# Performance work log

Measured on AMD Instinct MI355X. Metric: run time of the kernel, lower is better.

The kernel has to match this reference:

```python
import jax, jax.numpy as jnp
import numpy as np

RATIO_DENSE = 0.95   # ratio_th[-2] used for dense matching at conv5_2
RATIO_REFINE = 0.9   # ratio_th[k] used by refine_points
EPS = 1e-8
NEIGHBORS = jnp.array([[0, 0], [0, 1], [1, 0], [1, 1]])  # (x, y) offsets


def setup_inputs() -> dict:
    key = jax.random.key(0)
    k1, k2, k3, k4 = jax.random.split(key, 4)
    return {
        'map_A': jax.random.normal(k1, (1, 512, 96, 96), dtype=jnp.float32),
        'map_B': jax.random.normal(k2, (1, 512, 96, 96), dtype=jnp.float32),
        'act_A': jax.random.normal(k3, (1, 512, 192, 192), dtype=jnp.float32),
        'act_B': jax.random.normal(k4, (1, 512, 192, 192), dtype=jnp.float32),
    }


def _mnn_ratio_mask(sim, ratio):
    """Mutual-NN + ratio-test. sim: [N1, N2] cosine similarities.
    Returns nn12 [N1] (best match in B for each A) and boolean mask [N1]."""
    s12, i12 = jax.lax.top_k(sim, 2)            # [N1, 2]
    d12 = 2.0 - 2.0 * s12                       # cosine sim -> squared L2 dist
    r12 = d12[:, 0] / (d12[:, 1] + EPS)
    nn12 = i12[:, 0]
    s21, i21 = jax.lax.top_k(sim.T, 2)          # [N2, 2]
    d21 = 2.0 - 2.0 * s21
    r21 = d21[:, 0] / (d21[:, 1] + EPS)
    nn21 = i21[:, 0]
    ids1 = jnp.arange(sim.shape[0])
    mask = (ids1 == nn21[nn12]) & (r12 <= ratio) & (r21[nn12] <= ratio)
    return nn12, mask


def reference(map_A, map_B, act_A, act_B):
    ch = map_A.shape[1]
    hA, wA = map_A.shape[2], map_A.shape[3]
    hB, wB = map_B.shape[2], map_B.shape[3]

    # ---- dense_feature_matching (padded / masked form) ----
    d1 = map_A.reshape(ch, -1).T               # [N1, ch]
    d1 = d1 / jnp.linalg.norm(d1, axis=1, keepdims=True)
    d2 = map_B.reshape(ch, -1).T               # [N2, ch]
    d2 = d2 / jnp.linalg.norm(d2, axis=1, keepdims=True)
    sim = d1 @ d2.T                            # [N1, N2], the big one
    nn12, valid = _mnn_ratio_mask(sim, RATIO_DENSE)

    idx = jnp.arange(hA * wA)
    yA, xA = jnp.divmod(idx, wA)
    yB, xB = jnp.divmod(nn12, wB)
    border = ((xA == 0) | (xA == wA - 1) | (yA == 0) | (yA == hA - 1) |
              (xB == 0) | (xB == wB - 1) | (yB == 0) | (yB == hB - 1))
    valid = valid & ~border
    # pad invalid points to (0,0) so refine gathers stay in-bounds
    pA = jnp.stack([jnp.where(valid, xA, 0), jnp.where(valid, yA, 0)])  # [2, P]
    pB = jnp.stack([jnp.where(valid, xB, 0), jnp.where(valid, yB, 0)])

    # ---- refine_points (fully vectorized gather-dot-topk over all P points) ----
    dA = act_A[0] / jnp.sqrt(jnp.sum(act_A[0] ** 2, axis=0, keepdims=True))
    dB = act_B[0] / jnp.sqrt(jnp.sum(act_B[0] ** 2, axis=0, keepdims=True))
    pA2 = pA * 2
    pB2 = pB * 2
    P = pA.shape[1]

    gAx = pA2[0][:, None] + NEIGHBORS[:, 0][None, :]   # [P, 4]
    gAy = pA2[1][:, None] + NEIGHBORS[:, 1][None, :]
    gBx = pB2[0][:, None] + NEIGHBORS[:, 0][None, :]
    gBy = pB2[1][:, None] + NEIGHBORS[:, 1][None, :]
    actAg = dA[:, gAy, gAx]                            # [ch, P, 4]
    actBg = dB[:, gBy, gBx]                            # [ch, P, 4]
    scores = jnp.einsum('cpi,cpj->pij', actAg, actBg)  # [P, 4, 4]

    sA, mA = jax.lax.top_k(scores, 2)                  # [P, 4, 2]
    sA = 2.0 - 2.0 * sA
    ratio_A2B = sA[..., 0] / (sA[..., 1] + EPS)        # [P, 4]
    match_A2B = mA[..., 0]
    score_A2B = sA[..., 0]

    sB, mB = jax.lax.top_k(jnp.swapaxes(scores, 1, 2), 2)
    sB = 2.0 - 2.0 * sB
    ratio_B2A = sB[..., 0] / (sB[..., 1] + EPS)
    match_B2A = mB[..., 0]

    ar = jnp.arange(P)
    ind_A = (ar[:, None] * 4 + match_A2B).reshape(-1)  # [P*4]
    ind_B = (ar[:, None] * 4 + match_B2A).reshape(-1)
    ind = jnp.arange(P * 4)
    mask = (jnp.minimum(ratio_A2B, ratio_B2A) < RATIO_REFINE) & \
           (ind_B[ind_A] == ind).reshape(P, 4)

    # drop the two worst (largest-distance) neighbor candidates per point
    score_masked = jnp.where(mask, score_A2B, 5.0)
    _, discard = jax.lax.top_k(score_masked, 2)
    mask = mask.at[ar, discard[:, 0]].set(False)
    mask = mask.at[ar, discard[:, 1]].set(False)
    mask = mask & valid[:, None]

    refined_A = jnp.stack([gAx, gAy])                                   # [2, P, 4]
    rBx = pB2[0][:, None] + NEIGHBORS[:, 0][match_A2B]
    rBy = pB2[1][:, None] + NEIGHBORS[:, 1][match_A2B]
    refined_B = jnp.stack([rBx, rBy])                                   # [2, P, 4]

    return refined_A, refined_B, mask, scores
```

## Files before the change

### kernel.cpp

```cpp
#include <hip/hip_runtime.h>
#include <stdint.h>

#define CH 512
#define W1 96
#define P1 (W1*W1)
#define W2 192
#define P2 (W2*W2)
#define BM 256
#define BN 256
#define NTT 36
#define BK 32
#define NKS (CH/BK)
#define EPSF 1e-8f
#define RDENSE 0.95f
#define RREFINE 0.9f

typedef __attribute__((ext_vector_type(8))) short bf16x8_t;
typedef __attribute__((ext_vector_type(4))) float f32x4_t;

__device__ __forceinline__ unsigned enc_f32(float f){
  unsigned u = __float_as_uint(f);
  return (u & 0x80000000u) ? ~u : (u | 0x80000000u);
}
__device__ __forceinline__ float dec_f32(unsigned e){
  unsigned u = (e & 0x80000000u) ? (e & 0x7FFFFFFFu) : ~e;
  return __uint_as_float(u);
}
__device__ __forceinline__ unsigned long long packVI(float v, int idx){
  return (((unsigned long long)enc_f32(v)) << 32) | (unsigned)(~(unsigned)idx);
}
__device__ __forceinline__ float packedVal(unsigned long long p){ return dec_f32((unsigned)(p >> 32)); }
__device__ __forceinline__ int packedIdx(unsigned long long p){ return (int)(~(unsigned)(p & 0xFFFFFFFFull)); }
__device__ __forceinline__ void merge2(unsigned long long &b, unsigned long long &s, unsigned long long c){
  if (c > b){ s = b; b = c; } else if (c > s){ s = c; }
}

__device__ __forceinline__ unsigned short f2bf(float f){
  unsigned u = __float_as_uint(f);
  unsigned r = (u + 0x7FFFu + ((u >> 16) & 1u)) >> 16;
  return (unsigned short)r;
}

__device__ __forceinline__ void gload16(const void* g, void* l){
  __builtin_amdgcn_global_load_lds(
      (const __attribute__((address_space(1))) unsigned int*)g,
      (__attribute__((address_space(3))) unsigned int*)l, 16, 0, 0);
}

__global__ void desc_norm(const float* __restrict__ mA, const float* __restrict__ mB,
                          float* __restrict__ inv1, float* __restrict__ inv2){
  int p = blockIdx.x * blockDim.x + threadIdx.x;
  const float* m = (p < P1) ? mA : mB;
  float* o = (p < P1) ? inv1 : inv2;
  int pix = (p < P1) ? p : p - P1;
  float s = 0.f;
  for (int c = 0; c < CH; ++c){ float v = m[c*P1 + pix]; s += v*v; }
  o[pix] = 1.0f / sqrtf(s);
}

__global__ void act_norm(const float* __restrict__ aA, const float* __restrict__ aB,
                         float* __restrict__ invA, float* __restrict__ invB){
  int p = blockIdx.x * blockDim.x + threadIdx.x;
  const float* m = (p < P2) ? aA : aB;
  float* o = (p < P2) ? invA : invB;
  int pix = (p < P2) ? p : p - P2;
  float s = 0.f;
  for (int c = 0; c < CH; ++c){ float v = m[c*P2 + pix]; s += v*v; }
  o[pix] = 1.0f / sqrtf(s);
}

__global__ __launch_bounds__(256)
void prep_split(const float* __restrict__ src, const float* __restrict__ inv,
                unsigned short* __restrict__ hi, unsigned short* __restrict__ lo){
  __shared__ float tile[64][65];
  const int pixBase = blockIdx.x * 64;
  const int chBase  = blockIdx.y * 64;
  const int t = threadIdx.x;
  #pragma unroll
  for (int rep = 0; rep < 16; ++rep){
    int idx = rep*256 + t;
    int c = idx >> 6, p = idx & 63;
    tile[c][p] = src[(chBase + c)*P1 + pixBase + p];
  }
  __syncthreads();
  const int p = t >> 2, cg = (t & 3) * 16;
  const float iv = inv[pixBase + p];
  unsigned short hbuf[16], lbuf[16];
  #pragma unroll
  for (int j = 0; j < 16; ++j){
    float v = tile[cg + j][p] * iv;
    unsigned short h = f2bf(v);
    float hv = __uint_as_float((unsigned)h << 16);
    unsigned short l2 = f2bf(v - hv);
    hbuf[j] = h; lbuf[j] = l2;
  }
  size_t off = (size_t)(pixBase + p) * CH + chBase + cg;
  *(uint4*)(hi + off)     = ((const uint4*)hbuf)[0];
  *(uint4*)(hi + off + 8) = ((const uint4*)hbuf)[1];
  *(uint4*)(lo + off)     = ((const uint4*)lbuf)[0];
  *(uint4*)(lo + off + 8) = ((const uint4*)lbuf)[1];
}

__global__ __launch_bounds__(512, 2)
void sim_mfma(const unsigned short* __restrict__ Ah, const unsigned short* __restrict__ Al,
              const unsigned short* __restrict__ Bh, const unsigned short* __restrict__ Bl,
              unsigned long long* __restrict__ rowCand,
              unsigned long long* __restrict__ colCand){
  __shared__ __align__(16) char lds[131072];

  const int nwg = NTT*NTT;
  int bid = blockIdx.x;
  int swz = (bid & 7) * (nwg >> 3) + (bid >> 3);
  const int rt = swz / NTT, ct = swz % NTT;
  const int rBase = rt * BM, cBase = ct * BN;

  const int t = threadIdx.x;
  const int w = t >> 6, lane = t & 63;
  const int wr = w >> 2, wc = w & 3;
  const int l15 = lane & 15, lj = lane >> 4;

  const int panel = w >> 1, sub = w & 1;
  const unsigned short* gpan = (panel == 0) ? (Ah + (size_t)rBase*CH)
                             : (panel == 1) ? (Al + (size_t)rBase*CH)
                             : (panel == 2) ? (Bh + (size_t)cBase*CH)
                                            : (Bl + (size_t)cBase*CH);
  int gOff[8];
  #pragma unroll
  for (int i = 0; i < 8; ++i){
    int slot = sub*512 + i*64 + lane;
    int row = slot >> 2, chkp = slot & 3;
    int chk = chkp ^ ((row >> 1) & 3);
    gOff[i] = row * (CH*2) + chk * 16;
  }
  const int ldsPanelOff = panel*16384 + sub*8192;

  int aOff[8], bOff[4];
  #pragma unroll
  for (int mi = 0; mi < 8; ++mi){
    int rA = wr*128 + mi*16 + l15;
    aOff[mi] = rA*64 + ((lj ^ ((rA >> 1) & 3)) << 4);
  }
  #pragma unroll
  for (int ni = 0; ni < 4; ++ni){
    int rB = wc*64 + ni*16 + l15;
    bOff[ni] = rB*64 + ((lj ^ ((rB >> 1) & 3)) << 4);
  }

  f32x4_t acc[8][4];
  #pragma unroll
  for (int i = 0; i < 8; ++i)
    #pragma unroll
    for (int j = 0; j < 4; ++j)
      #pragma unroll
      for (int r = 0; r < 4; ++r) acc[i][j][r] = 0.f;

  {
    const char* gb = (const char*)gpan;
    #pragma unroll
    for (int i = 0; i < 8; ++i)
      gload16(gb + gOff[i], lds + ldsPanelOff + i*1024);
  }
  __syncthreads();

  for (int ks = 0; ks < NKS; ++ks){
    const int cur = ks & 1;
    if (ks + 1 < NKS){
      const char* gb = (const char*)gpan + (ks+1)*BK*2;
      #pragma unroll
      for (int i = 0; i < 8; ++i)
        gload16(gb + gOff[i], lds + (cur^1)*65536 + ldsPanelOff + i*1024);
    }
    const char* bp = lds + cur*65536;
    bf16x8_t ahf[8], alf[8];
    #pragma unroll
    for (int mi = 0; mi < 8; ++mi){
      ahf[mi] = *(const bf16x8_t*)(bp + aOff[mi]);
      alf[mi] = *(const bf16x8_t*)(bp + 16384 + aOff[mi]);
    }
    #pragma unroll
    for (int ni = 0; ni < 4; ++ni){
      bf16x8_t bhf = *(const bf16x8_t*)(bp + 32768 + bOff[ni]);
      bf16x8_t blf = *(const bf16x8_t*)(bp + 49152 + bOff[ni]);
      #pragma unroll
      for (int mi = 0; mi < 8; ++mi){
        acc[mi][ni] = __builtin_amdgcn_mfma_f32_16x16x32_bf16(ahf[mi], bhf, acc[mi][ni], 0, 0, 0);
        acc[mi][ni] = __builtin_amdgcn_mfma_f32_16x16x32_bf16(ahf[mi], blf, acc[mi][ni], 0, 0, 0);
        acc[mi][ni] = __builtin_amdgcn_mfma_f32_16x16x32_bf16(alf[mi], bhf, acc[mi][ni], 0, 0, 0);
      }
    }
    __syncthreads();
  }

  unsigned long long (*rowScr)[4][2] = (unsigned long long (*)[4][2])(lds);
  unsigned long long (*colScr)[2][2] = (unsigned long long (*)[2][2])(lds + 16384);

  #pragma unroll
  for (int mi = 0; mi < 8; ++mi){
    #pragma unroll
    for (int reg = 0; reg < 4; ++reg){
      unsigned long long b = 0ull, s = 0ull;
      #pragma unroll
      for (int ni = 0; ni < 4; ++ni){
        int col = cBase + wc*64 + ni*16 + l15;
        merge2(b, s, packVI(acc[mi][ni][reg], col));
      }
      #pragma unroll
      for (int m = 1; m < 16; m <<= 1){
        unsigned long long ob = __shfl_xor(b, m, 64);
        unsigned long long os = __shfl_xor(s, m, 64);
        merge2(b, s, ob); merge2(b, s, os);
      }
      if (l15 == 0){
        int rowLoc = wr*128 + mi*16 + lj*4 + reg;
        rowScr[rowLoc][wc][0] = b; rowScr[rowLoc][wc][1] = s;
      }
    }
  }
  #pragma unroll
  for (int ni = 0; ni < 4; ++ni){
    unsigned long long b = 0ull, s = 0ull;
    #pragma unroll
    for (int mi = 0; mi < 8; ++mi)
      #pragma unroll
      for (int reg = 0; reg < 4; ++reg){
        int row = rBase + wr*128 + mi*16 + lj*4 + reg;
        merge2(b, s, packVI(acc[mi][ni][reg], row));
      }
    #pragma unroll
    for (int m = 16; m < 64; m <<= 1){
      unsigned long long ob = __shfl_xor(b, m, 64);
      unsigned long long os = __shfl_xor(s, m, 64);
      merge2(b, s, ob); merge2(b, s, os);
    }
    if (lj == 0){
      int colLoc = wc*64 + ni*16 + l15;
      colScr[colLoc][wr][0] = b; colScr[colLoc][wr][1] = s;
    }
  }
  __syncthreads();
  if (t < 256){
    unsigned long long b = 0ull, s = 0ull;
    #pragma unroll
    for (int j = 0; j < 4; ++j){ merge2(b, s, rowScr[t][j][0]); merge2(b, s, rowScr[t][j][1]); }
    rowCand[((long long)ct*P1 + rBase + t)*2 + 0] = b;
    rowCand[((long long)ct*P1 + rBase + t)*2 + 1] = s;
  } else {
    int c = t - 256;
    unsigned long long b = 0ull, s = 0ull;
    #pragma unroll
    for (int j = 0; j < 2; ++j){ merge2(b, s, colScr[c][j][0]); merge2(b, s, colScr[c][j][1]); }
    colCand[((long long)rt*P1 + cBase + c)*2 + 0] = b;
    colCand[((long long)rt*P1 + cBase + c)*2 + 1] = s;
  }
}

__global__ void merge_cand(const unsigned long long* __restrict__ cand,
                           unsigned long long* __restrict__ top,
                           unsigned long long* __restrict__ sec){
  int p = blockIdx.x * blockDim.x + threadIdx.x;
  unsigned long long b = 0ull, s = 0ull;
  for (int tile = 0; tile < NTT; ++tile){
    merge2(b, s, cand[((long long)tile*P1 + p)*2 + 0]);
    merge2(b, s, cand[((long long)tile*P1 + p)*2 + 1]);
  }
  top[p] = b; sec[p] = s;
}

__global__ void match_k(const unsigned long long* __restrict__ rowTop,
                        const unsigned long long* __restrict__ rowSec,
                        const unsigned long long* __restrict__ colTop,
                        const unsigned long long* __restrict__ colSec,
                        int4* __restrict__ pts, int* __restrict__ validArr){
  int p = blockIdx.x * blockDim.x + threadIdx.x;
  unsigned long long rT = rowTop[p], rS = rowSec[p];
  float s0 = packedVal(rT), s1 = packedVal(rS);
  int nn12 = packedIdx(rT);
  float r12 = (2.f - 2.f*s0) / (2.f - 2.f*s1 + EPSF);
  unsigned long long cT = colTop[nn12], cS = colSec[nn12];
  int nn21 = packedIdx(cT);
  float r21 = (2.f - 2.f*packedVal(cT)) / (2.f - 2.f*packedVal(cS) + EPSF);
  int xA = p % W1, yA = p / W1, xB = nn12 % W1, yB = nn12 / W1;
  bool border = (xA==0)||(xA==W1-1)||(yA==0)||(yA==W1-1)||
                (xB==0)||(xB==W1-1)||(yB==0)||(yB==W1-1);
  bool valid = (nn21 == p) && (r12 <= RDENSE) && (r21 <= RDENSE) && !border;
  pts[p] = valid ? make_int4(xA,yA,xB,yB) : make_int4(0,0,0,0);
  validArr[p] = valid ? 1 : 0;
}

__global__ __launch_bounds__(256)
void refine(const float* __restrict__ actA, const float* __restrict__ actB,
            const float* __restrict__ invA, const float* __restrict__ invB,
            const int4* __restrict__ pts, float* __restrict__ scoresOut){
  int p = (blockIdx.x * blockDim.x + threadIdx.x) >> 6;
  int lane = threadIdx.x & 63;
  int4 q = pts[p];
  const int nbx[4] = {0,0,1,1}, nby[4] = {0,1,0,1};
  int offA[4], offB[4];
  #pragma unroll
  for (int i = 0; i < 4; ++i){
    offA[i] = (2*q.y + nby[i])*W2 + 2*q.x + nbx[i];
    offB[i] = (2*q.w + nby[i])*W2 + 2*q.z + nbx[i];
  }
  float acc[16] = {};
  #pragma unroll
  for (int k = 0; k < 8; ++k){
    int c = lane + 64*k;
    int base = c * P2;
    float a0 = actA[base+offA[0]], a1 = actA[base+offA[1]],
          a2 = actA[base+offA[2]], a3 = actA[base+offA[3]];
    float b0 = actB[base+offB[0]], b1 = actB[base+offB[1]],
          b2 = actB[base+offB[2]], b3 = actB[base+offB[3]];
    acc[ 0] = fmaf(a0,b0,acc[ 0]); acc[ 1] = fmaf(a0,b1,acc[ 1]);
    acc[ 2] = fmaf(a0,b2,acc[ 2]); acc[ 3] = fmaf(a0,b3,acc[ 3]);
    acc[ 4] = fmaf(a1,b0,acc[ 4]); acc[ 5] = fmaf(a1,b1,acc[ 5]);
    acc[ 6] = fmaf(a1,b2,acc[ 6]); acc[ 7] = fmaf(a1,b3,acc[ 7]);
    acc[ 8] = fmaf(a2,b0,acc[ 8]); acc[ 9] = fmaf(a2,b1,acc[ 9]);
    acc[10] = fmaf(a2,b2,acc[10]); acc[11] = fmaf(a2,b3,acc[11]);
    acc[12] = fmaf(a3,b0,acc[12]); acc[13] = fmaf(a3,b1,acc[13]);
    acc[14] = fmaf(a3,b2,acc[14]); acc[15] = fmaf(a3,b3,acc[15]);
  }
  #pragma unroll
  for (int m = 1; m < 64; m <<= 1)
    #pragma unroll
    for (int u = 0; u < 16; ++u) acc[u] += __shfl_xor(acc[u], m, 64);
  if (lane == 0){
    float sA[4], sB[4];
    #pragma unroll
    for (int i = 0; i < 4; ++i){ sA[i] = invA[offA[i]]; sB[i] = invB[offB[i]]; }
    float4* o = (float4*)(scoresOut + p*16);
    #pragma unroll
    for (int i = 0; i < 4; ++i)
      o[i] = make_float4(acc[i*4+0]*sA[i]*sB[0], acc[i*4+1]*sA[i]*sB[1],
                         acc[i*4+2]*sA[i]*sB[2], acc[i*4+3]*sA[i]*sB[3]);
  }
}

__global__ void final_k(const float* __restrict__ scores, const int4* __restrict__ pts,
                        const int* __restrict__ validArr, float* __restrict__ out){
  int p = blockIdx.x * blockDim.x + threadIdx.x;
  float sc[16];
  #pragma unroll
  for (int u = 0; u < 16; ++u) sc[u] = scores[p*16 + u];

  int matchA[4]; float ratioA[4], scoreA[4];
  #pragma unroll
  for (int i = 0; i < 4; ++i){
    int bi = 0; float bv = sc[i*4];
    #pragma unroll
    for (int j = 1; j < 4; ++j) if (sc[i*4+j] > bv){ bv = sc[i*4+j]; bi = j; }
    float sv = -3.402823466e38f;
    #pragma unroll
    for (int j = 0; j < 4; ++j) if (j != bi && sc[i*4+j] > sv){ sv = sc[i*4+j]; }
    matchA[i] = bi;
    float d0 = 2.f - 2.f*bv, d1 = 2.f - 2.f*sv;
    ratioA[i] = d0 / (d1 + EPSF); scoreA[i] = d0;
  }
  int matchB[4]; float ratioB[4];
  #pragma unroll
  for (int j = 0; j < 4; ++j){
    int bi = 0; float bv = sc[j];
    #pragma unroll
    for (int i = 1; i < 4; ++i) if (sc[i*4+j] > bv){ bv = sc[i*4+j]; bi = i; }
    float sv = -3.402823466e38f;
    #pragma unroll
    for (int i = 0; i < 4; ++i) if (i != bi && sc[i*4+j] > sv){ sv = sc[i*4+j]; }
    matchB[j] = bi;
    float d0 = 2.f - 2.f*bv, d1 = 2.f - 2.f*sv;
    ratioB[j] = d0 / (d1 + EPSF);
  }
  bool m[4];
  #pragma unroll
  for (int i = 0; i < 4; ++i)
    m[i] = (fminf(ratioA[i], ratioB[i]) < RREFINE) && (matchB[matchA[i]] == i);
  float smk[4];
  #pragma unroll
  for (int i = 0; i < 4; ++i) smk[i] = m[i] ? scoreA[i] : 5.0f;
  int d0i = 0; float d0v = smk[0];
  #pragma unroll
  for (int i = 1; i < 4; ++i) if (smk[i] > d0v){ d0v = smk[i]; d0i = i; }
  int d1i = -1; float d1v = -3.402823466e38f;
  #pragma unroll
  for (int i = 0; i < 4; ++i) if (i != d0i && smk[i] > d1v){ d1v = smk[i]; d1i = i; }
  m[d0i] = false; m[d1i] = false;
  bool v = validArr[p] != 0;
  int4 q = pts[p];
  const int nbx[4] = {0,0,1,1}, nby[4] = {0,1,0,1};
  #pragma unroll
  for (int i = 0; i < 4; ++i){
    out[           p*4 + i] = (float)(2*q.x + nbx[i]);
    out[  P1*4   + p*4 + i] = (float)(2*q.y + nby[i]);
    out[2*P1*4   + p*4 + i] = (float)(2*q.z + nbx[matchA[i]]);
    out[3*P1*4   + p*4 + i] = (float)(2*q.w + nby[matchA[i]]);
    out[4*P1*4   + p*4 + i] = (m[i] && v) ? 1.0f : 0.0f;
  }
}

extern "C" void kernel_launch(void* const* d_in, const int* in_sizes, int n_in,
                              void* d_out, int out_size, void* d_ws, size_t ws_size,
                              hipStream_t stream) {
  const float* mapA = (const float*)d_in[0];
  const float* mapB = (const float*)d_in[1];
  const float* actA = (const float*)d_in[2];
  const float* actB = (const float*)d_in[3];
  float* out = (float*)d_out;

  unsigned short* Ah = (unsigned short*)d_ws;
  unsigned short* Al = Ah + (size_t)P1*CH;
  unsigned short* Bh = Al + (size_t)P1*CH;
  unsigned short* Bl = Bh + (size_t)P1*CH;
  unsigned long long* rowCand = (unsigned long long*)(Bl + (size_t)P1*CH);
  unsigned long long* colCand = rowCand + (size_t)NTT*P1*2;
  unsigned long long* rowTop  = colCand + (size_t)NTT*P1*2;
  unsigned long long* rowSec  = rowTop + P1;
  unsigned long long* colTop  = rowSec + P1;
  unsigned long long* colSec  = colTop + P1;
  float* inv1 = (float*)(colSec + P1);
  float* inv2 = inv1 + P1;
  float* invA = inv2 + P1;
  float* invB = invA + P2;
  int4*  pts  = (int4*)(invB + P2);
  int*   validArr = (int*)(pts + P1);

  float* scoresOut = out + 4*P1*4 + P1*4;

  desc_norm <<<2*P1/256, 256, 0, stream>>>(mapA, mapB, inv1, inv2);
  act_norm  <<<2*P2/256, 256, 0, stream>>>(actA, actB, invA, invB);
  prep_split<<<dim3(P1/64, CH/64), 256, 0, stream>>>(mapA, inv1, Ah, Al);
  prep_split<<<dim3(P1/64, CH/64), 256, 0, stream>>>(mapB, inv2, Bh, Bl);
  sim_mfma  <<<NTT*NTT, 512, 0, stream>>>(Ah, Al, Bh, Bl, rowCand, colCand);
  merge_cand<<<P1/256, 256, 0, stream>>>(rowCand, rowTop, rowSec);
  merge_cand<<<P1/256, 256, 0, stream>>>(colCand, colTop, colSec);
  match_k   <<<P1/256, 256, 0, stream>>>(rowTop, rowSec, colTop, colSec, pts, validArr);
  refine    <<<P1*64/256, 256, 0, stream>>>(actA, actB, invA, invB, pts, scoresOut);
  final_k   <<<P1/256, 256, 0, stream>>>(scoresOut, pts, validArr, out);
}
```

Before: 1.762 ms.

## Pre-swizzle GEMM operands into K-blocked layout and transpose activations for refine

prep_split now writes the bf16 hi/lo descriptors in a K-blocked (32-channel slab), pre-swizzled layout. The GEMM's global-to-LDS loads therefore become contiguous per panel, with no per-thread offset tables. The GEMM MFMA section is also wrapped in s_setprio to favour math waves. Refine gets an optional path that transposes the full activation tensors to pixel-major so per-point gathers become contiguous vector loads, at the cost of an extra full pass over about 150MB of activations. That path only runs when the workspace is large enough.

```diff
diff --git a/kernel.cpp b/kernel.cpp
--- a/kernel.cpp
+++ b/kernel.cpp
@@ -65,7 +65,7 @@
   float* o = (p < P2) ? invA : invB;
   int pix = (p < P2) ? p : p - P2;
   float s = 0.f;
-  for (int c = 0; c < CH; ++c){ float v = m[c*P2 + pix]; s += v*v; }
+  for (int c = 0; c < CH; ++c){ float v = m[(size_t)c*P2 + pix]; s += v*v; }
   o[pix] = 1.0f / sqrtf(s);
 }
 
@@ -84,21 +84,26 @@
   }
   __syncthreads();
   const int p = t >> 2, cg = (t & 3) * 16;
-  const float iv = inv[pixBase + p];
+  const int pix = pixBase + p;
+  const float iv = inv[pix];
   unsigned short hbuf[16], lbuf[16];
   #pragma unroll
   for (int j = 0; j < 16; ++j){
     float v = tile[cg + j][p] * iv;
     unsigned short h = f2bf(v);
     float hv = __uint_as_float((unsigned)h << 16);
-    unsigned short l2 = f2bf(v - hv);
-    hbuf[j] = h; lbuf[j] = l2;
-  }
-  size_t off = (size_t)(pixBase + p) * CH + chBase + cg;
-  *(uint4*)(hi + off)     = ((const uint4*)hbuf)[0];
-  *(uint4*)(hi + off + 8) = ((const uint4*)hbuf)[1];
-  *(uint4*)(lo + off)     = ((const uint4*)lbuf)[0];
-  *(uint4*)(lo + off + 8) = ((const uint4*)lbuf)[1];
+    lbuf[j] = f2bf(v - hv);
+    hbuf[j] = h;
+  }
+  const int c0 = chBase + cg;
+  const int kb = c0 >> 5;
+  const int ck0 = (c0 & 31) >> 3;
+  const int sz = (pix >> 1) & 3;
+  size_t base = (size_t)kb*(P1*32) + (size_t)pix*32;
+  *(uint4*)(hi + base + ((ck0    ^sz)<<3)) = ((const uint4*)hbuf)[0];
+  *(uint4*)(hi + base + (((ck0+1)^sz)<<3)) = ((const uint4*)hbuf)[1];
+  *(uint4*)(lo + base + ((ck0    ^sz)<<3)) = ((const uint4*)lbuf)[0];
+  *(uint4*)(lo + base + (((ck0+1)^sz)<<3)) = ((const uint4*)lbuf)[1];
 }
 
 __global__ __launch_bounds__(512, 2)
@@ -120,19 +125,10 @@
   const int l15 = lane & 15, lj = lane >> 4;
 
   const int panel = w >> 1, sub = w & 1;
-  const unsigned short* gpan = (panel == 0) ? (Ah + (size_t)rBase*CH)
-                             : (panel == 1) ? (Al + (size_t)rBase*CH)
-                             : (panel == 2) ? (Bh + (size_t)cBase*CH)
-                                            : (Bl + (size_t)cBase*CH);
-  int gOff[8];
-  #pragma unroll
-  for (int i = 0; i < 8; ++i){
-    int slot = sub*512 + i*64 + lane;
-    int row = slot >> 2, chkp = slot & 3;
-    int chk = chkp ^ ((row >> 1) & 3);
-    gOff[i] = row * (CH*2) + chk * 16;
-  }
-  const int ldsPanelOff = panel*16384 + sub*8192;
+  const unsigned short* pptr = (panel==0)?Ah:(panel==1)?Al:(panel==2)?Bh:Bl;
+  const int Base = (panel < 2) ? rBase : cBase;
+  const char* gpan = (const char*)pptr + (size_t)Base*64 + sub*8192;
+  char* ldsPan0 = lds + panel*16384 + sub*8192;
 
   int aOff[8], bOff[4];
   #pragma unroll
@@ -154,21 +150,19 @@
       #pragma unroll
       for (int r = 0; r < 4; ++r) acc[i][j][r] = 0.f;
 
-  {
-    const char* gb = (const char*)gpan;
-    #pragma unroll
-    for (int i = 0; i < 8; ++i)
-      gload16(gb + gOff[i], lds + ldsPanelOff + i*1024);
-  }
+  #pragma unroll
+  for (int i = 0; i < 8; ++i)
+    gload16(gpan + i*1024 + lane*16, ldsPan0 + i*1024);
   __syncthreads();
 
   for (int ks = 0; ks < NKS; ++ks){
     const int cur = ks & 1;
     if (ks + 1 < NKS){
-      const char* gb = (const char*)gpan + (ks+1)*BK*2;
+      const char* gb = gpan + (size_t)(ks+1)*(P1*64);
+      char* lb = ldsPan0 + (cur^1)*65536;
       #pragma unroll
       for (int i = 0; i < 8; ++i)
-        gload16(gb + gOff[i], lds + (cur^1)*65536 + ldsPanelOff + i*1024);
+        gload16(gb + i*1024 + lane*16, lb + i*1024);
     }
     const char* bp = lds + cur*65536;
     bf16x8_t ahf[8], alf[8];
@@ -177,6 +171,7 @@
       ahf[mi] = *(const bf16x8_t*)(bp + aOff[mi]);
       alf[mi] = *(const bf16x8_t*)(bp + 16384 + aOff[mi]);
     }
+    __builtin_amdgcn_s_setprio(1);
     #pragma unroll
     for (int ni = 0; ni < 4; ++ni){
       bf16x8_t bhf = *(const bf16x8_t*)(bp + 32768 + bOff[ni]);
@@ -188,6 +183,7 @@
         acc[mi][ni] = __builtin_amdgcn_mfma_f32_16x16x32_bf16(alf[mi], bhf, acc[mi][ni], 0, 0, 0);
       }
     }
+    __builtin_amdgcn_s_setprio(0);
     __syncthreads();
   }
 
@@ -288,6 +284,80 @@
 }
 
 __global__ __launch_bounds__(256)
+void act_transpose(const float* __restrict__ aA, const float* __restrict__ aB,
+                   float* __restrict__ tA, float* __restrict__ tB){
+  __shared__ float tile[64][65];
+  const int pixBase = blockIdx.x * 64;
+  const int chBase  = blockIdx.y * 64;
+  const float* src = blockIdx.z ? aB : aA;
+  float*       dst = blockIdx.z ? tB : tA;
+  const int t = threadIdx.x;
+  #pragma unroll
+  for (int rep = 0; rep < 16; ++rep){
+    int idx = rep*256 + t;
+    int c = idx >> 6, p = idx & 63;
+    tile[c][p] = src[(size_t)(chBase + c)*P2 + pixBase + p];
+  }
+  __syncthreads();
+  const int p = t >> 2, cg = (t & 3) * 16;
+  size_t base = (size_t)(pixBase + p)*CH + chBase + cg;
+  #pragma unroll
+  for (int q = 0; q < 4; ++q){
+    float4 v = make_float4(tile[cg+q*4+0][p], tile[cg+q*4+1][p],
+                           tile[cg+q*4+2][p], tile[cg+q*4+3][p]);
+    *(float4*)(dst + base + q*4) = v;
+  }
+}
+
+__global__ __launch_bounds__(256)
+void refine_t(const float* __restrict__ tA, const float* __restrict__ tB,
+              const float* __restrict__ invA, const float* __restrict__ invB,
+              const int4* __restrict__ pts, float* __restrict__ scoresOut){
+  int p = (blockIdx.x * blockDim.x + threadIdx.x) >> 6;
+  int lane = threadIdx.x & 63;
+  int4 q = pts[p];
+  const int nbx[4] = {0,0,1,1}, nby[4] = {0,1,0,1};
+  int offA[4], offB[4];
+  #pragma unroll
+  for (int i = 0; i < 4; ++i){
+    offA[i] = (2*q.y + nby[i])*W2 + 2*q.x + nbx[i];
+    offB[i] = (2*q.w + nby[i])*W2 + 2*q.z + nbx[i];
+  }
+  float a[4][8], b[4][8];
+  #pragma unroll
+  for (int i = 0; i < 4; ++i){
+    const float* pa = tA + (size_t)offA[i]*CH + lane*8;
+    *(float4*)&a[i][0] = *(const float4*)pa;
+    *(float4*)&a[i][4] = *(const float4*)(pa + 4);
+    const float* pb = tB + (size_t)offB[i]*CH + lane*8;
+    *(float4*)&b[i][0] = *(const float4*)pb;
+    *(float4*)&b[i][4] = *(const float4*)(pb + 4);
+  }
+  float acc[16] = {};
+  #pragma unroll
+  for (int ch = 0; ch < 8; ++ch)
+    #pragma unroll
+    for (int i = 0; i < 4; ++i)
+      #pragma unroll
+      for (int j = 0; j < 4; ++j)
+        acc[i*4+j] = fmaf(a[i][ch], b[j][ch], acc[i*4+j]);
+  #pragma unroll
+  for (int m = 1; m < 64; m <<= 1)
+    #pragma unroll
+    for (int u = 0; u < 16; ++u) acc[u] += __shfl_xor(acc[u], m, 64);
+  if (lane == 0){
+    float sA[4], sB[4];
+    #pragma unroll
+    for (int i = 0; i < 4; ++i){ sA[i] = invA[offA[i]]; sB[i] = invB[offB[i]]; }
+    float4* o = (float4*)(scoresOut + p*16);
+    #pragma unroll
+    for (int i = 0; i < 4; ++i)
+      o[i] = make_float4(acc[i*4+0]*sA[i]*sB[0], acc[i*4+1]*sA[i]*sB[1],
+                         acc[i*4+2]*sA[i]*sB[2], acc[i*4+3]*sA[i]*sB[3]);
+  }
+}
+
+__global__ __launch_bounds__(256)
 void refine(const float* __restrict__ actA, const float* __restrict__ actB,
             const float* __restrict__ invA, const float* __restrict__ invB,
             const int4* __restrict__ pts, float* __restrict__ scoresOut){
@@ -305,7 +375,7 @@
   #pragma unroll
   for (int k = 0; k < 8; ++k){
     int c = lane + 64*k;
-    int base = c * P2;
+    size_t base = (size_t)c * P2;
     float a0 = actA[base+offA[0]], a1 = actA[base+offA[1]],
           a2 = actA[base+offA[2]], a3 = actA[base+offA[3]];
     float b0 = actB[base+offB[0]], b1 = actB[base+offB[1]],
@@ -420,6 +490,10 @@
   float* invB = invA + P2;
   int4*  pts  = (int4*)(invB + P2);
   int*   validArr = (int*)(pts + P1);
+  float* tA = (float*)(validArr + P1);
+  float* tB = tA + (size_t)P2*CH;
+  size_t needBytes = (size_t)((char*)(tB + (size_t)P2*CH) - (char*)d_ws);
+  const bool useT = ws_size >= needBytes;
 
   float* scoresOut = out + 4*P1*4 + P1*4;
 
@@ -431,6 +505,11 @@
   merge_cand<<<P1/256, 256, 0, stream>>>(rowCand, rowTop, rowSec);
   merge_cand<<<P1/256, 256, 0, stream>>>(colCand, colTop, colSec);
   match_k   <<<P1/256, 256, 0, stream>>>(rowTop, rowSec, colTop, colSec, pts, validArr);
-  refine    <<<P1*64/256, 256, 0, stream>>>(actA, actB, invA, invB, pts, scoresOut);
+  if (useT){
+    act_transpose<<<dim3(P2/64, CH/64, 2), 256, 0, stream>>>(actA, actB, tA, tB);
+    refine_t <<<P1*64/256, 256, 0, stream>>>(tA, tB, invA, invB, pts, scoresOut);
+  } else {
+    refine   <<<P1*64/256, 256, 0, stream>>>(actA, actB, invA, invB, pts, scoresOut);
+  }
   final_k   <<<P1/256, 256, 0, stream>>>(scoresOut, pts, validArr, out);
 }
```

Measured after the change: 1.764 ms. Within noise of the previous version (+0.1%).
